# Kernel optimization log

Measured on AMD Instinct MI355X. Metric: run time of the kernel, lower is better.

The kernel has to match this reference:

```python
import jax, jax.numpy as jnp
import numpy as np
import jax.scipy.signal as jss

SX, SY, C, K = 256, 256, 3, 10
C0 = [0, 0, 0, 1, 1, 1, 2, 2, 2, 0]
C1 = [[0, 1, 2, 9], [3, 4, 5], [6, 7, 8]]
DD, DT, SIGMA = 5, 0.2, 0.65

_KX = jnp.array([[-1., 0., 1.], [-2., 0., 2.], [-1., 0., 1.]])
_KY = _KX.T


def _conv2(A, Kf):
    # zero-padded 'same' 2D true convolution, vmapped over channel axis
    return jax.vmap(lambda a: jss.convolve2d(a, Kf, mode='same'), in_axes=2, out_axes=2)(A)


def sobel(A):
    # (X, Y, c) -> (X, Y, 2, c): [sobel_y, sobel_x] stacked on axis 2 (FlowLenia convention)
    return jnp.concatenate([_conv2(A, _KY)[:, :, None, :], _conv2(A, _KX)[:, :, None, :]], axis=2)


def growth(U, m, s):
    # bell(U,m,s)*2 - 1
    return jnp.exp(-((U - m) / s) ** 2 / 2.) * 2. - 1.


def get_kernels_fft(R, r, a, w, b):
    # FlowLenia kernel construction: ring distance -> smooth cutoff * sum-of-bumps, normalized, fft2(fftshift)
    mid = SX // 2
    xs = jnp.arange(-mid, mid, dtype=jnp.float32)
    D = jnp.sqrt(xs[:, None] ** 2 + xs[None, :] ** 2)            # (X, Y)
    Dk = D[..., None] / ((R + 15.) * r)                          # (X, Y, k)
    ker = (b * jnp.exp(-(Dk[..., None] - a) ** 2 / w)).sum(-1)   # (X, Y, k)
    sig = 0.5 * (jnp.tanh(-(Dk - 1.) * 10. / 2.) + 1.)           # sigmoid(-(D-1)*10)
    Kk = sig * ker
    nK = Kk / Kk.sum(axis=(0, 1), keepdims=True)
    return jnp.fft.fft2(jnp.fft.fftshift(nK, axes=(0, 1)), axes=(0, 1))


def _rt_apply(A, F):
    # Reintegration tracking with 'wall' border: flow-driven mass redistribution over a (2dd+1)^2 neighborhood
    ii = jnp.arange(SX, dtype=jnp.float32)
    pos = jnp.stack(jnp.meshgrid(ii, ii, indexing='ij'), axis=-1) + 0.5   # (X, Y, 2) cell centers
    ma = DD - SIGMA                                   # max flow magnitude
    mu = pos[..., None] + jnp.clip(DT * F, -ma, ma)   # (X, Y, 2, C) target centers
    mu = jnp.clip(mu, SIGMA, SX - SIGMA)              # wall border
    offs = jnp.arange(-DD, DD + 1)
    gx, gy = jnp.meshgrid(offs, offs, indexing='ij')
    dxs, dys = gx.reshape(-1), gy.reshape(-1)
    clip_hi = min(1., 2. * SIGMA)

    def step(dx, dy):
        Ar = jnp.roll(A, (dx, dy), axis=(0, 1))
        mur = jnp.roll(mu, (dx, dy), axis=(0, 1))
        dpmu = jnp.abs(pos[..., None] - mur)                                  # (X, Y, 2, C)
        sz = 0.5 - dpmu + SIGMA
        area = jnp.prod(jnp.clip(sz, 0., clip_hi), axis=2) / (4. * SIGMA ** 2)  # (X, Y, C)
        return Ar * area

    return jax.vmap(step)(dxs, dys).sum(axis=0)


def setup_inputs() -> dict:
    key = jax.random.key(0)
    ks = jax.random.split(key, 9)
    A = jax.random.uniform(ks[0], (SX, SY, C), dtype=jnp.float32)
    R = jax.random.uniform(ks[1], (), minval=2.0, maxval=25.0)
    r = jax.random.uniform(ks[2], (K,), minval=0.2, maxval=1.0)
    m = jax.random.uniform(ks[3], (K,), minval=0.05, maxval=0.5)
    s = jax.random.uniform(ks[4], (K,), minval=0.001, maxval=0.18)
    h = jax.random.uniform(ks[5], (K,), minval=0.01, maxval=1.0)
    a = jax.random.uniform(ks[6], (K, 3), minval=0.0, maxval=1.0)
    b = jax.random.uniform(ks[7], (K, 3), minval=0.001, maxval=1.0)
    w = jax.random.uniform(ks[8], (K, 3), minval=0.01, maxval=0.5)
    return dict(A=A, R=R, r=r, m=m, s=s, h=h, a=a, b=b, w=w)


def reference(A, R, r, m, s, h, a, b, w):
    fK = get_kernels_fft(R, r, a, w, b)                       # (X, Y, k) complex
    fA = jnp.fft.fft2(A, axes=(0, 1))
    fAk = fA[:, :, jnp.array(C0)]                             # (X, Y, k)
    U = jnp.real(jnp.fft.ifft2(fK * fAk, axes=(0, 1)))        # (X, Y, k)
    U = growth(U, m, s) * h
    U = jnp.dstack([U[:, :, C1[c]].sum(axis=-1) for c in range(C)])  # (X, Y, C)
    nabla_U = sobel(U)                                        # (X, Y, 2, C)
    nabla_A = sobel(A.sum(axis=-1, keepdims=True))            # (X, Y, 2, 1)
    alpha = jnp.clip((A[:, :, None, :] / C) ** 2, 0., 1.)     # (X, Y, 1, C)
    F = nabla_U * (1. - alpha) - nabla_A * alpha              # (X, Y, 2, C)
    return _rt_apply(A, F)
```

## Files before the change

kernel.cpp:

```cpp
#include <hip/hip_runtime.h>

#define NPIX 65536

#define OX1ARE(c) ((0  + (c))*NPIX)
#define OX1AIM(c) ((3  + (c))*NPIX)
#define OX1K(k)   ((6  + (k))*NPIX)
#define OX2ARE(c) ((16 + (c))*NPIX)
#define OX2AIM(c) ((19 + (c))*NPIX)
#define OX2K(k)   ((22 + (k))*NPIX)
#define OX3RE(j)  ((32 + (j))*NPIX)
#define OX3IM(j)  ((37 + (j))*NPIX)
#define OU(k)     ((42 + (k))*NPIX)
#define OPACK(c)  ((52 + 4*(c))*NPIX)
#define OROWS     (64*NPIX)

__device__ __forceinline__ void fft256_core(float* __restrict__ re, float* __restrict__ im,
                                            const float* __restrict__ twr,
                                            const float* __restrict__ twi, int lane) {
    #pragma unroll
    for (int s = 1; s <= 8; ++s) {
        int h = 1 << (s - 1);
        #pragma unroll
        for (int b = 0; b < 2; ++b) {
            int idx = b*64 + lane;
            int pos = idx & (h - 1);
            int g   = idx >> (s - 1);
            int i0 = (g << s) + pos;
            int i1 = i0 + h;
            int tj = pos << (8 - s);
            float wr = twr[tj], wi = twi[tj];
            float xr = re[i1], xi = im[i1];
            float br = fmaf(xr, wr, -xi*wi);
            float bi = fmaf(xr, wi,  xi*wr);
            float ar = re[i0], ai = im[i0];
            re[i0] = ar + br; im[i0] = ai + bi;
            re[i1] = ar - br; im[i1] = ai - bi;
        }
    }
}

__device__ __forceinline__ void build_tw(float* twr, float* twi, int t, float sgn) {
    if (t < 128) {
        float ang = (float)t * 0.0245436930f;
        twr[t] = cosf(ang);
        twi[t] = sgn * sinf(ang);
    }
}

__device__ __forceinline__ void store_t4(float* __restrict__ dst, const float* __restrict__ buf,
                                         int off, int t, int lb) {
    float4 v;
    v.x = buf[0*512 + off + t];
    v.y = buf[1*512 + off + t];
    v.z = buf[2*512 + off + t];
    v.w = buf[3*512 + off + t];
    *(float4*)&dst[t*256 + lb] = v;
}

struct KP { float rden, a0,a1,a2, b0,b1,b2, iw0,iw1,iw2; };

__device__ __forceinline__ void load_kp(KP& kp, int k, float R,
        const float* __restrict__ r_, const float* __restrict__ a_,
        const float* __restrict__ b_, const float* __restrict__ w_) {
    kp.rden = 1.0f / ((R + 15.0f) * r_[k]);
    kp.a0 = a_[k*3+0]; kp.a1 = a_[k*3+1]; kp.a2 = a_[k*3+2];
    kp.b0 = b_[k*3+0]; kp.b1 = b_[k*3+1]; kp.b2 = b_[k*3+2];
    kp.iw0 = 1.0f/w_[k*3+0]; kp.iw1 = 1.0f/w_[k*3+1]; kp.iw2 = 1.0f/w_[k*3+2];
}

__device__ __forceinline__ float kval(int di, int dj, const KP& kp) {
    float D  = sqrtf((float)(di*di + dj*dj));
    float Dk = D * kp.rden;
    if (Dk > 3.0f) return 0.0f;
    float d0 = Dk - kp.a0, d1 = Dk - kp.a1, d2 = Dk - kp.a2;
    float ker = kp.b0*expf(-(d0*d0)*kp.iw0)
              + kp.b1*expf(-(d1*d1)*kp.iw1)
              + kp.b2*expf(-(d2*d2)*kp.iw2);
    float sig = 1.0f / (1.0f + expf(10.0f*(Dk - 1.0f)));
    return sig * ker;
}

__global__ __launch_bounds__(256) void fwd_rows(const float* __restrict__ A,
        const float* __restrict__ R_, const float* __restrict__ r_,
        const float* __restrict__ a_, const float* __restrict__ b_,
        const float* __restrict__ w_, float* __restrict__ ws) {
    __shared__ float buf[4*512];
    __shared__ float twr[128], twi[128];
    int p  = blockIdx.x >> 6;
    int lb = (blockIdx.x & 63) * 4;
    int wid = threadIdx.x >> 6, lane = threadIdx.x & 63;
    int t = threadIdx.x;
    build_tw(twr, twi, t, -1.0f);
    int iw = lb + wid;
    float* re = &buf[wid*512];
    float* im = re + 256;

    int fa, fb;
    switch (p) {
        case 0:  fa = 0;  fb = 1;  break;
        case 1:  fa = 2;  fb = 12; break;
        case 2:  fa = 3;  fb = 4;  break;
        case 3:  fa = 5;  fb = 6;  break;
        case 4:  fa = 7;  fb = 8;  break;
        case 5:  fa = 9;  fb = 10; break;
        default: fa = 11; fb = -1; break;
    }
    bool aA = (fa < 3);
    bool bA = (fb >= 0 && fb < 3);
    float R = R_[0];
    int di = ((iw + 128) & 255) - 128;
    KP kpa, kpb;
    if (!aA)      load_kp(kpa, fa - 3, R, r_, a_, b_, w_);
    if (fb >= 3)  load_kp(kpb, fb - 3, R, r_, a_, b_, w_);
    float sum_a = 0.0f, sum_b = 0.0f;
    #pragma unroll
    for (int e = 0; e < 4; ++e) {
        int idx = e*64 + lane;
        int dst = __brev(idx) >> 24;
        int dj  = ((idx + 128) & 255) - 128;
        float vf, vg;
        if (aA) vf = A[(iw*256 + idx)*3 + fa];
        else    { vf = kval(di, dj, kpa); sum_a += vf; }
        if (fb < 0)      vg = 0.0f;
        else if (bA)     vg = A[(iw*256 + idx)*3 + fb];
        else             { vg = kval(di, dj, kpb); sum_b += vg; }
        re[dst] = vf;
        im[dst] = vg;
    }
    if (!aA) {
        float s = sum_a;
        #pragma unroll
        for (int off = 32; off; off >>= 1) s += __shfl_xor(s, off);
        if (lane == 0) ws[OROWS + (fa - 3)*256 + iw] = s;
    }
    if (fb >= 3) {
        float s = sum_b;
        #pragma unroll
        for (int off = 32; off; off >>= 1) s += __shfl_xor(s, off);
        if (lane == 0) ws[OROWS + (fb - 3)*256 + iw] = s;
    }
    __syncthreads();
    fft256_core(re, im, twr, twi, lane);
    __syncthreads();
    if (t <= 128) {
        if (p <= 1) {
            int u2 = (256 - t) & 255;
            float4 Fre, Fim, Gre, Gim;
            float* pF[4] = {&Fre.x, &Fim.x, &Gre.x, &Gim.x};
            #pragma unroll
            for (int l = 0; l < 4; ++l) {
                float zr1 = buf[l*512 + t],  zi1 = buf[l*512 + 256 + t];
                float zr2 = buf[l*512 + u2], zi2 = buf[l*512 + 256 + u2];
                pF[0][l] = 0.5f*(zr1 + zr2);
                pF[1][l] = 0.5f*(zi1 - zi2);
                pF[2][l] = 0.5f*(zi1 + zi2);
                pF[3][l] = 0.5f*(zr2 - zr1);
            }
            if (p == 0) {
                *(float4*)&ws[OX1ARE(0) + t*256 + lb] = Fre;
                *(float4*)&ws[OX1AIM(0) + t*256 + lb] = Fim;
                *(float4*)&ws[OX1ARE(1) + t*256 + lb] = Gre;
                *(float4*)&ws[OX1AIM(1) + t*256 + lb] = Gim;
            } else {
                *(float4*)&ws[OX1ARE(2) + t*256 + lb] = Fre;
                *(float4*)&ws[OX1AIM(2) + t*256 + lb] = Fim;
                *(float4*)&ws[OX1K(9)   + t*256 + lb] = Gre;
            }
        } else {
            float4 va, vb;
            float* pV[2] = {&va.x, &vb.x};
            #pragma unroll
            for (int l = 0; l < 4; ++l) {
                pV[0][l] = buf[l*512 + t];
                pV[1][l] = buf[l*512 + 256 + t];
            }
            *(float4*)&ws[OX1K(fa - 3) + t*256 + lb] = va;
            if (fb >= 0) *(float4*)&ws[OX1K(fb - 3) + t*256 + lb] = vb;
        }
    }
}

__global__ __launch_bounds__(256) void fwd_cols(float* __restrict__ ws) {
    __shared__ float buf[4*512];
    __shared__ float twr[128], twi[128];
    __shared__ float kks[2];
    int bid = blockIdx.x;
    int wid = threadIdx.x >> 6, lane = threadIdx.x & 63;
    int t = threadIdx.x;
    build_tw(twr, twi, t, -1.0f);
    float* re = &buf[wid*512];
    float* im = re + 256;
    if (bid < 99) {
        int c  = bid / 33;
        int ub = (bid % 33) * 4;
        int u  = ub + wid; if (u > 128) u = 128;
        const float* rr = ws + OX1ARE(c) + u*256;
        const float* ri = ws + OX1AIM(c) + u*256;
        #pragma unroll
        for (int e = 0; e < 4; ++e) {
            int idx = e*64 + lane;
            int dst = __brev(idx) >> 24;
            re[dst] = rr[idx];
            im[dst] = ri[idx];
        }
        __syncthreads();
        fft256_core(re, im, twr, twi, lane);
        __syncthreads();
        store_t4(ws + OX2ARE(c), buf, 0,   t, ub);
        store_t4(ws + OX2AIM(c), buf, 256, t, ub);
    } else {
        int q  = (bid - 99) / 33;
        int ub = ((bid - 99) % 33) * 4;
        int u  = ub + wid; if (u > 128) u = 128;
        if (wid < 2) {
            const float* rw = ws + OROWS + (2*q + wid)*256;
            float v = rw[lane] + rw[64+lane] + rw[128+lane] + rw[192+lane];
            #pragma unroll
            for (int off = 32; off; off >>= 1) v += __shfl_xor(v, off);
            if (lane == 0) kks[wid] = 1.0f / (v * 65536.0f);
        }
        const float* ra = ws + OX1K(2*q)     + u*256;
        const float* rb = ws + OX1K(2*q + 1) + u*256;
        #pragma unroll
        for (int e = 0; e < 4; ++e) {
            int idx = e*64 + lane;
            int dst = __brev(idx) >> 24;
            re[dst] = ra[idx];
            im[dst] = rb[idx];
        }
        __syncthreads();
        fft256_core(re, im, twr, twi, lane);
        __syncthreads();
        if (t <= 128) {
            float sa = kks[0], sb = kks[1];
            float4 va, vb;
            va.x = buf[0*512 + t]*sa;  vb.x = buf[0*512 + 256 + t]*sb;
            va.y = buf[1*512 + t]*sa;  vb.y = buf[1*512 + 256 + t]*sb;
            va.z = buf[2*512 + t]*sa;  vb.z = buf[2*512 + 256 + t]*sb;
            va.w = buf[3*512 + t]*sa;  vb.w = buf[3*512 + 256 + t]*sb;
            *(float4*)&ws[OX2K(2*q)     + t*256 + ub] = va;
            *(float4*)&ws[OX2K(2*q + 1) + t*256 + ub] = vb;
        }
    }
}

__global__ __launch_bounds__(256) void inv_rows(float* __restrict__ ws) {
    __shared__ float buf[4*512];
    __shared__ float twr[128], twi[128];
    int j  = blockIdx.x >> 6;
    int lb = (blockIdx.x & 63) * 4;
    int wid = threadIdx.x >> 6, lane = threadIdx.x & 63;
    int t = threadIdx.x;
    build_tw(twr, twi, t, 1.0f);
    int ka = 2*j, kb = 2*j + 1;
    int ca = (ka < 9) ? ka/3 : 0;
    int cb = (kb < 9) ? kb/3 : 0;
    int v  = lb + wid;
    int vr = (256 - v) & 255;
    int vf = (v <= 128) ? v : 256 - v;
    const float* Aare_v = ws + OX2ARE(ca) + v*256;
    const float* Aaim_v = ws + OX2AIM(ca) + v*256;
    const float* Aare_r = ws + OX2ARE(ca) + vr*256;
    const float* Aaim_r = ws + OX2AIM(ca) + vr*256;
    const float* Bare_v = ws + OX2ARE(cb) + v*256;
    const float* Baim_v = ws + OX2AIM(cb) + v*256;
    const float* Bare_r = ws + OX2ARE(cb) + vr*256;
    const float* Baim_r = ws + OX2AIM(cb) + vr*256;
    const float* Ka = ws + OX2K(ka) + vf*256;
    const float* Kb = ws + OX2K(kb) + vf*256;
    float* re = &buf[wid*512];
    float* im = re + 256;
    #pragma unroll
    for (int e = 0; e < 4; ++e) {
        int idx = e*64 + lane;
        int dst = __brev(idx) >> 24;
        bool hi = idx > 128;
        int uf = hi ? 256 - idx : idx;
        const float* pAr = hi ? Aare_r : Aare_v;
        const float* pAi = hi ? Aaim_r : Aaim_v;
        const float* pBr = hi ? Bare_r : Bare_v;
        const float* pBi = hi ? Baim_r : Baim_v;
        float ar = pAr[uf];
        float ai = pAi[uf]; ai = hi ? -ai : ai;
        float br = pBr[uf];
        float bi = pBi[uf]; bi = hi ? -bi : bi;
        float kva = Ka[uf], kvb = Kb[uf];
        float uar = ar*kva, uai = ai*kva;
        float ubr = br*kvb, ubi = bi*kvb;
        re[dst] = uar - ubi;
        im[dst] = uai + ubr;
    }
    __syncthreads();
    fft256_core(re, im, twr, twi, lane);
    __syncthreads();
    store_t4(ws + OX3RE(j), buf, 0,   t, lb);
    store_t4(ws + OX3IM(j), buf, 256, t, lb);
}

__global__ __launch_bounds__(256) void inv_cols(float* __restrict__ ws,
                                                const float* __restrict__ m_,
                                                const float* __restrict__ s_,
                                                const float* __restrict__ h_) {
    __shared__ float buf[4*512];
    __shared__ float twr[128], twi[128];
    int j  = blockIdx.x >> 6;
    int lb = (blockIdx.x & 63) * 4;
    int wid = threadIdx.x >> 6, lane = threadIdx.x & 63;
    int t = threadIdx.x;
    build_tw(twr, twi, t, 1.0f);
    float* re = &buf[wid*512];
    float* im = re + 256;
    const float* rr = ws + OX3RE(j) + (lb + wid)*256;
    const float* ri = ws + OX3IM(j) + (lb + wid)*256;
    #pragma unroll
    for (int e = 0; e < 4; ++e) {
        int idx = e*64 + lane;
        int dst = __brev(idx) >> 24;
        re[dst] = rr[idx];
        im[dst] = ri[idx];
    }
    __syncthreads();
    fft256_core(re, im, twr, twi, lane);
    __syncthreads();
    int k0 = 2*j, k1 = 2*j + 1;
    float m0 = m_[k0], m1 = m_[k1];
    float c0 = 0.5f/(s_[k0]*s_[k0]), c1 = 0.5f/(s_[k1]*s_[k1]);
    float h0 = h_[k0], h1 = h_[k1];
    float4 va, vb;
    #pragma unroll
    for (int l = 0; l < 4; ++l) {
        float u0 = buf[l*512 + t]       - m0;
        float u1 = buf[l*512 + 256 + t] - m1;
        (&va.x)[l] = h0 * fmaf(2.0f, expf(-(u0*u0)*c0), -1.0f);
        (&vb.x)[l] = h1 * fmaf(2.0f, expf(-(u1*u1)*c1), -1.0f);
    }
    *(float4*)&ws[OU(k0) + t*256 + lb] = va;
    *(float4*)&ws[OU(k1) + t*256 + lb] = vb;
}

__global__ __launch_bounds__(256) void growth_mu(const float* __restrict__ A,
                                                 float* __restrict__ ws) {
    __shared__ float Gs[3][256];
    __shared__ float As[3][256];
    int b = blockIdx.x;
    int c = b >> 8;
    int x = b & 255;
    int t = threadIdx.x;
    int nk = (c == 0) ? 4 : 3;
    #pragma unroll
    for (int rr = 0; rr < 3; ++rr) {
        int xr = x - 1 + rr;
        float sv = 0.0f, gv = 0.0f;
        if (xr >= 0 && xr <= 255) {
            int idx = xr*256 + t;
            int base = idx*3;
            sv = A[base] + A[base + 1] + A[base + 2];
            for (int kk = 0; kk < nk; ++kk) {
                int k = (kk == 3) ? 9 : c*3 + kk;
                gv += ws[OU(k) + idx];
            }
        }
        As[rr][t] = sv;
        Gs[rr][t] = gv;
    }
    __syncthreads();
    int y = t;
    float vA[3][3], vU[3][3];
    #pragma unroll
    for (int ii = 0; ii < 3; ++ii)
        #pragma unroll
        for (int jj = 0; jj < 3; ++jj) {
            int yy = y - 1 + jj;
            bool ok = (yy >= 0 && yy <= 255);
            vA[ii][jj] = ok ? As[ii][yy] : 0.0f;
            vU[ii][jj] = ok ? Gs[ii][yy] : 0.0f;
        }
    float gyA = (vA[0][0] + 2.0f*vA[0][1] + vA[0][2]) - (vA[2][0] + 2.0f*vA[2][1] + vA[2][2]);
    float gxA = (vA[0][0] + 2.0f*vA[1][0] + vA[2][0]) - (vA[0][2] + 2.0f*vA[1][2] + vA[2][2]);
    float gy  = (vU[0][0] + 2.0f*vU[0][1] + vU[0][2]) - (vU[2][0] + 2.0f*vU[2][1] + vU[2][2]);
    float gx  = (vU[0][0] + 2.0f*vU[1][0] + vU[2][0]) - (vU[0][2] + 2.0f*vU[1][2] + vU[2][2]);
    float a = A[(x*256 + y)*3 + c];
    float al = (a / 3.0f); al = al * al;
    al = fminf(fmaxf(al, 0.0f), 1.0f);
    float F0 = gy * (1.0f - al) - gyA * al;
    float F1 = gx * (1.0f - al) - gxA * al;
    float d0 = fminf(fmaxf(0.2f * F0, -4.35f), 4.35f);
    float d1 = fminf(fmaxf(0.2f * F1, -4.35f), 4.35f);
    float mux = fminf(fmaxf((float)x + 0.5f + d0, 0.65f), 255.35f);
    float muy = fminf(fmaxf((float)y + 0.5f + d1, 0.65f), 255.35f);
    float4 pk;
    pk.x = a;
    pk.y = mux - ((float)x + 0.5f);
    pk.z = muy;
    pk.w = 0.0f;
    *(float4*)&ws[OPACK(c) + (x*256 + y)*4] = pk;
}

__global__ __launch_bounds__(256) void rt_scatter(const float* __restrict__ ws,
                                                  float* __restrict__ out) {
    __shared__ float acc[256];
    int b = blockIdx.x;
    int c = b >> 8;
    int x = b & 255;
    int t = threadIdx.x;
    acc[t] = 0.0f;
    __syncthreads();
    const float4* pp = (const float4*)&ws[OPACK(c)];
    #pragma unroll
    for (int i = 0; i < 11; ++i) {
        int s = i - 5;
        int xs = (x - s) & 255;
        float dxf = (float)(x - xs);
        float4 v = pp[xs*256 + t];
        float wx = __builtin_amdgcn_fmed3f(1.15f - fabsf(dxf - v.y), 0.0f, 1.0f);
        float wxa = v.x * wx;
        if (wxa != 0.0f) {
            int by = (int)ceilf(v.z - 1.65f);
            float fy = (float)by + 0.5f - v.z;
            #pragma unroll
            for (int q = 0; q < 3; ++q) {
                float ay = __builtin_amdgcn_fmed3f(1.15f - fabsf(fy + (float)q), 0.0f, 1.0f);
                atomicAdd(&acc[(by + q) & 255], wxa * ay);
            }
        }
    }
    __syncthreads();
    out[(x*256 + t)*3 + c] = acc[t] * (1.0f / (4.0f * 0.65f * 0.65f));
}

extern "C" void kernel_launch(void* const* d_in, const int* in_sizes, int n_in,
                              void* d_out, int out_size, void* d_ws, size_t ws_size,
                              hipStream_t stream) {
    const float* A = (const float*)d_in[0];
    const float* R = (const float*)d_in[1];
    const float* r = (const float*)d_in[2];
    const float* m = (const float*)d_in[3];
    const float* s = (const float*)d_in[4];
    const float* h = (const float*)d_in[5];
    const float* a = (const float*)d_in[6];
    const float* b = (const float*)d_in[7];
    const float* w = (const float*)d_in[8];
    float* ws  = (float*)d_ws;
    float* out = (float*)d_out;

    fwd_rows<<<7*64, 256, 0, stream>>>(A, R, r, a, b, w, ws);
    fwd_cols<<<99 + 165, 256, 0, stream>>>(ws);
    inv_rows<<<5*64, 256, 0, stream>>>(ws);
    inv_cols<<<5*64, 256, 0, stream>>>(ws, m, s, h);
    growth_mu<<<768, 256, 0, stream>>>(A, ws);
    rt_scatter<<<768, 256, 0, stream>>>(ws, out);
}
```

Baseline: 113.7 us.

## Fuse flow computation into reintegration scatter kernel with recomputed halo rows

Merges the growth/Sobel/flow kernel and the reintegration scatter kernel into one. Each block loads a 13-row halo of the summed growth field and mass into shared memory and recomputes the flow for the 11 source rows it needs, instead of writing and re-reading a packed float4 intermediate. This removes one launch and the intermediate global round trip. In exchange each block does about 11x the Sobel/flow arithmetic and about 4x more global loads for its halo rows.

```diff
diff --git a/kernel.cpp b/kernel.cpp
--- a/kernel.cpp
+++ b/kernel.cpp
@@ -11,8 +11,7 @@
 #define OX3RE(j)  ((32 + (j))*NPIX)
 #define OX3IM(j)  ((37 + (j))*NPIX)
 #define OU(k)     ((42 + (k))*NPIX)
-#define OPACK(c)  ((52 + 4*(c))*NPIX)
-#define OROWS     (64*NPIX)
+#define OROWS     (52*NPIX)
 
 __device__ __forceinline__ void fft256_core(float* __restrict__ re, float* __restrict__ im,
                                             const float* __restrict__ twr,
@@ -338,18 +337,20 @@
     *(float4*)&ws[OU(k1) + t*256 + lb] = vb;
 }
 
-__global__ __launch_bounds__(256) void growth_mu(const float* __restrict__ A,
-                                                 float* __restrict__ ws) {
-    __shared__ float Gs[3][256];
-    __shared__ float As[3][256];
+__global__ __launch_bounds__(256) void growth_rt(const float* __restrict__ A,
+                                                 const float* __restrict__ ws,
+                                                 float* __restrict__ out) {
+    __shared__ float Gs[13][256];
+    __shared__ float As[13][256];
+    __shared__ float acc[256];
     int b = blockIdx.x;
     int c = b >> 8;
     int x = b & 255;
     int t = threadIdx.x;
     int nk = (c == 0) ? 4 : 3;
-    #pragma unroll
-    for (int rr = 0; rr < 3; ++rr) {
-        int xr = x - 1 + rr;
+    acc[t] = 0.0f;
+    for (int i = 0; i < 13; ++i) {
+        int xr = x - 6 + i;
         float sv = 0.0f, gv = 0.0f;
         if (xr >= 0 && xr <= 255) {
             int idx = xr*256 + t;
@@ -360,63 +361,46 @@
                 gv += ws[OU(k) + idx];
             }
         }
-        As[rr][t] = sv;
-        Gs[rr][t] = gv;
+        As[i][t] = sv;
+        Gs[i][t] = gv;
     }
     __syncthreads();
     int y = t;
-    float vA[3][3], vU[3][3];
-    #pragma unroll
-    for (int ii = 0; ii < 3; ++ii)
-        #pragma unroll
-        for (int jj = 0; jj < 3; ++jj) {
-            int yy = y - 1 + jj;
-            bool ok = (yy >= 0 && yy <= 255);
-            vA[ii][jj] = ok ? As[ii][yy] : 0.0f;
-            vU[ii][jj] = ok ? Gs[ii][yy] : 0.0f;
-        }
-    float gyA = (vA[0][0] + 2.0f*vA[0][1] + vA[0][2]) - (vA[2][0] + 2.0f*vA[2][1] + vA[2][2]);
-    float gxA = (vA[0][0] + 2.0f*vA[1][0] + vA[2][0]) - (vA[0][2] + 2.0f*vA[1][2] + vA[2][2]);
-    float gy  = (vU[0][0] + 2.0f*vU[0][1] + vU[0][2]) - (vU[2][0] + 2.0f*vU[2][1] + vU[2][2]);
-    float gx  = (vU[0][0] + 2.0f*vU[1][0] + vU[2][0]) - (vU[0][2] + 2.0f*vU[1][2] + vU[2][2]);
-    float a = A[(x*256 + y)*3 + c];
-    float al = (a / 3.0f); al = al * al;
-    al = fminf(fmaxf(al, 0.0f), 1.0f);
-    float F0 = gy * (1.0f - al) - gyA * al;
-    float F1 = gx * (1.0f - al) - gxA * al;
-    float d0 = fminf(fmaxf(0.2f * F0, -4.35f), 4.35f);
-    float d1 = fminf(fmaxf(0.2f * F1, -4.35f), 4.35f);
-    float mux = fminf(fmaxf((float)x + 0.5f + d0, 0.65f), 255.35f);
-    float muy = fminf(fmaxf((float)y + 0.5f + d1, 0.65f), 255.35f);
-    float4 pk;
-    pk.x = a;
-    pk.y = mux - ((float)x + 0.5f);
-    pk.z = muy;
-    pk.w = 0.0f;
-    *(float4*)&ws[OPACK(c) + (x*256 + y)*4] = pk;
-}
-
-__global__ __launch_bounds__(256) void rt_scatter(const float* __restrict__ ws,
-                                                  float* __restrict__ out) {
-    __shared__ float acc[256];
-    int b = blockIdx.x;
-    int c = b >> 8;
-    int x = b & 255;
-    int t = threadIdx.x;
-    acc[t] = 0.0f;
-    __syncthreads();
-    const float4* pp = (const float4*)&ws[OPACK(c)];
     #pragma unroll
     for (int i = 0; i < 11; ++i) {
-        int s = i - 5;
-        int xs = (x - s) & 255;
-        float dxf = (float)(x - xs);
-        float4 v = pp[xs*256 + t];
-        float wx = __builtin_amdgcn_fmed3f(1.15f - fabsf(dxf - v.y), 0.0f, 1.0f);
-        float wxa = v.x * wx;
+        int xr = x - 5 + i;
+        if (xr < 0 || xr > 255) continue;
+        int ri = i + 1;
+        float vA[3][3], vU[3][3];
+        #pragma unroll
+        for (int ii = 0; ii < 3; ++ii)
+            #pragma unroll
+            for (int jj = 0; jj < 3; ++jj) {
+                int yy = y - 1 + jj;
+                bool ok = (yy >= 0 && yy <= 255);
+                vA[ii][jj] = ok ? As[ri - 1 + ii][yy] : 0.0f;
+                vU[ii][jj] = ok ? Gs[ri - 1 + ii][yy] : 0.0f;
+            }
+        float gyA = (vA[0][0] + 2.0f*vA[0][1] + vA[0][2]) - (vA[2][0] + 2.0f*vA[2][1] + vA[2][2]);
+        float gxA = (vA[0][0] + 2.0f*vA[1][0] + vA[2][0]) - (vA[0][2] + 2.0f*vA[1][2] + vA[2][2]);
+        float gy  = (vU[0][0] + 2.0f*vU[0][1] + vU[0][2]) - (vU[2][0] + 2.0f*vU[2][1] + vU[2][2]);
+        float gx  = (vU[0][0] + 2.0f*vU[1][0] + vU[2][0]) - (vU[0][2] + 2.0f*vU[1][2] + vU[2][2]);
+        float a = A[(xr*256 + y)*3 + c];
+        float al = (a / 3.0f); al = al * al;
+        al = fminf(fmaxf(al, 0.0f), 1.0f);
+        float F0 = gy * (1.0f - al) - gyA * al;
+        float F1 = gx * (1.0f - al) - gxA * al;
+        float d0 = fminf(fmaxf(0.2f * F0, -4.35f), 4.35f);
+        float d1 = fminf(fmaxf(0.2f * F1, -4.35f), 4.35f);
+        float mux = fminf(fmaxf((float)xr + 0.5f + d0, 0.65f), 255.35f);
+        float muy = fminf(fmaxf((float)y  + 0.5f + d1, 0.65f), 255.35f);
+        float dxp = mux - ((float)xr + 0.5f);
+        float dxf = (float)(x - xr);
+        float wx  = __builtin_amdgcn_fmed3f(1.15f - fabsf(dxf - dxp), 0.0f, 1.0f);
+        float wxa = a * wx;
         if (wxa != 0.0f) {
-            int by = (int)ceilf(v.z - 1.65f);
-            float fy = (float)by + 0.5f - v.z;
+            int by = (int)ceilf(muy - 1.65f);
+            float fy = (float)by + 0.5f - muy;
             #pragma unroll
             for (int q = 0; q < 3; ++q) {
                 float ay = __builtin_amdgcn_fmed3f(1.15f - fabsf(fy + (float)q), 0.0f, 1.0f);
@@ -447,6 +431,5 @@
     fwd_cols<<<99 + 165, 256, 0, stream>>>(ws);
     inv_rows<<<5*64, 256, 0, stream>>>(ws);
     inv_cols<<<5*64, 256, 0, stream>>>(ws, m, s, h);
-    growth_mu<<<768, 256, 0, stream>>>(A, ws);
-    rt_scatter<<<768, 256, 0, stream>>>(ws, out);
-}
+    growth_rt<<<768, 256, 0, stream>>>(A, ws, out);
+}
```

New measurement: 117.8 us. +3.6%, slower.
